# Optimization experiments

Hardware: AMD Instinct MI355X
Metric: run time of the kernel (lower is better)

Reference implementation:

```python
import jax, jax.numpy as jnp
import numpy as np

PI = float(np.pi)


def setup_inputs() -> dict:
    key = jax.random.key(0)
    k1, k2 = jax.random.split(key)
    src = jax.random.normal(k1, (32, 4, 512, 512), dtype=jnp.float32)
    fc2 = jax.random.normal(k2, (32, 7), dtype=jnp.float32)
    return {"src": src, "fc2": fc2}


def _build_mat(fc2):
    # Parameter extraction exactly as in the torch module.
    theta = jnp.clip(fc2[:, 0] * 0.3, -1.0, 1.0) * PI          # rotation angle
    scale = jnp.clip(fc2[:, 1:3] * 0.3 + 1.0, 0.0, 5.0)
    trans = fc2[:, 3:5] * 0.3
    shear = jnp.clip(fc2[:, 5:7] * 0.3, -1.0, 1.0) * PI
    sx, sy = scale[:, 0], scale[:, 1]
    tx, ty = trans[:, 0], trans[:, 1]
    shxy, shyx = shear[:, 0], shear[:, 1]
    c, s = jnp.cos(theta), jnp.sin(theta)
    z, o = jnp.zeros_like(c), jnp.ones_like(c)

    def m3(rows):  # rows: list of 3 lists of 3 (B,) scalars -> (B,3,3)
        return jnp.stack([jnp.stack(r, axis=-1) for r in rows], axis=-2)

    # Note: the torch code stacks rows at dim=2 (making the transpose) then
    # transposes (1,2) back, so the effective matrices are the ones as-written.
    rot = m3([[c, -s, z], [s, c, z], [z, z, o]])
    scl = m3([[sx, z, z], [z, sy, z], [z, z, o]])
    shr = m3([[o, shxy, z], [shyx, o, z], [z, z, o]])
    trn = m3([[o, z, tx], [z, o, ty], [z, z, o]])
    # mat = T @ Sh @ S @ R  (batched 3x3 matmuls)
    return trn @ shr @ scl @ rot


def _affine_grid(theta2x3, H, W):
    # F.affine_grid with align_corners=False (the torch default used here):
    # pixel centers map to x=(2w+1)/W-1, y=(2h+1)/H-1.
    xs = (2.0 * jnp.arange(W, dtype=jnp.float32) + 1.0) / W - 1.0  # (W,)
    ys = (2.0 * jnp.arange(H, dtype=jnp.float32) + 1.0) / H - 1.0  # (H,)
    base = jnp.stack([
        jnp.broadcast_to(xs[None, :], (H, W)),
        jnp.broadcast_to(ys[:, None], (H, W)),
        jnp.ones((H, W), dtype=jnp.float32),
    ], axis=-1)                                                     # (H,W,3)
    return jnp.einsum('bij,hwj->bhwi', theta2x3, base)              # (B,H,W,2)


def _grid_sample(src, grid):
    # bilinear, padding_mode='zeros', align_corners=False
    B, C, H, W = src.shape
    ix = ((grid[..., 0] + 1.0) * W - 1.0) * 0.5  # (B,H,W) source x coords
    iy = ((grid[..., 1] + 1.0) * H - 1.0) * 0.5
    x0 = jnp.floor(ix)
    y0 = jnp.floor(iy)
    wx = ix - x0  # frac weights
    wy = iy - y0
    x0i = x0.astype(jnp.int32)
    y0i = y0.astype(jnp.int32)

    def gather(img, xi, yi):  # img (C,H,W); xi,yi (H,W) int
        valid = ((xi >= 0) & (xi < W) & (yi >= 0) & (yi < H)).astype(img.dtype)
        v = img[:, jnp.clip(yi, 0, H - 1), jnp.clip(xi, 0, W - 1)]  # (C,H,W)
        return v * valid[None]

    def per_batch(img, x0i, y0i, wx, wy):
        v00 = gather(img, x0i, y0i)
        v01 = gather(img, x0i + 1, y0i)
        v10 = gather(img, x0i, y0i + 1)
        v11 = gather(img, x0i + 1, y0i + 1)
        return (v00 * (1 - wx) * (1 - wy) + v01 * wx * (1 - wy)
                + v10 * (1 - wx) * wy + v11 * wx * wy)

    return jax.vmap(per_batch)(src, x0i, y0i, wx, wy)


def reference(src, fc2):
    H, W = src.shape[2], src.shape[3]
    mat = _build_mat(fc2)                     # (B,3,3)
    inv_mat = jnp.linalg.inv(mat)             # (B,3,3)
    grid = _affine_grid(mat[:, :2, :], H, W)
    inv_grid = _affine_grid(inv_mat[:, :2, :], H, W)
    transformed = _grid_sample(src, grid)
    return transformed, mat, inv_mat, grid, inv_grid
```

## Files before the change

### kernel.cpp

```cpp
#include <hip/hip_runtime.h>

#define PI_F 3.14159265358979323846f

typedef float f32x4 __attribute__((ext_vector_type(4)));

__global__ void build_mats_kernel(const float* __restrict__ fc2,
                                  float* __restrict__ mat_out,
                                  float* __restrict__ inv_out,
                                  int B) {
    int b = blockIdx.x * blockDim.x + threadIdx.x;
    if (b >= B) return;
    const float* f = fc2 + b * 7;
    float theta = fminf(fmaxf(f[0] * 0.3f, -1.f), 1.f) * PI_F;
    float sx    = fminf(fmaxf(f[1] * 0.3f + 1.f, 0.f), 5.f);
    float sy    = fminf(fmaxf(f[2] * 0.3f + 1.f, 0.f), 5.f);
    float tx    = f[3] * 0.3f;
    float ty    = f[4] * 0.3f;
    float shxy  = fminf(fmaxf(f[5] * 0.3f, -1.f), 1.f) * PI_F;
    float shyx  = fminf(fmaxf(f[6] * 0.3f, -1.f), 1.f) * PI_F;

    float c = cosf(theta), s = sinf(theta);
    float m00 =  sx * c + shxy * sy * s;
    float m01 = -sx * s + shxy * sy * c;
    float m02 = tx;
    float m10 = shyx * sx * c + sy * s;
    float m11 = -shyx * sx * s + sy * c;
    float m12 = ty;

    float* m = mat_out + b * 9;
    m[0] = m00; m[1] = m01; m[2] = m02;
    m[3] = m10; m[4] = m11; m[5] = m12;
    m[6] = 0.f; m[7] = 0.f; m[8] = 1.f;

    float det = m00 * m11 - m01 * m10;
    float id  = 1.f / det;
    float i00 =  m11 * id, i01 = -m01 * id;
    float i10 = -m10 * id, i11 =  m00 * id;
    float i02 = -(i00 * m02 + i01 * m12);
    float i12 = -(i10 * m02 + i11 * m12);

    float* im = inv_out + b * 9;
    im[0] = i00; im[1] = i01; im[2] = i02;
    im[3] = i10; im[4] = i11; im[5] = i12;
    im[6] = 0.f; im[7] = 0.f; im[8] = 1.f;
}

__global__ __launch_bounds__(256) void grid_kernel(
    const float* __restrict__ mat,
    const float* __restrict__ inv_mat,
    float* __restrict__ grid_out,
    float* __restrict__ inv_grid_out)
{
    const int W = 512, H = 512;
    const int h = blockIdx.x;
    const int b = blockIdx.y;
    const int w = threadIdx.x * 2;

    float xs0 = (2.f * (float)w + 1.f) * (1.f / (float)W) - 1.f;
    float xs1 = xs0 + 2.f / (float)W;
    float ys  = (2.f * (float)h + 1.f) * (1.f / (float)H) - 1.f;

    const float* m  = mat + b * 9;
    const float* im = inv_mat + b * 9;

    float gx0  = m[0] * xs0 + (m[1] * ys + m[2]);
    float gy0  = m[3] * xs0 + (m[4] * ys + m[5]);
    float gx1  = m[0] * xs1 + (m[1] * ys + m[2]);
    float gy1  = m[3] * xs1 + (m[4] * ys + m[5]);
    float igx0 = im[0] * xs0 + (im[1] * ys + im[2]);
    float igy0 = im[3] * xs0 + (im[4] * ys + im[5]);
    float igx1 = im[0] * xs1 + (im[1] * ys + im[2]);
    float igy1 = im[3] * xs1 + (im[4] * ys + im[5]);

    size_t vec = ((size_t)b * H + h) * (W / 2) + threadIdx.x;
    f32x4 g  = {gx0, gy0, gx1, gy1};
    f32x4 ig = {igx0, igy0, igx1, igy1};
    __builtin_nontemporal_store(g,  (f32x4*)grid_out + vec);
    __builtin_nontemporal_store(ig, (f32x4*)inv_grid_out + vec);
}

__global__ __launch_bounds__(256) void sample_kernel(
    const float* __restrict__ src,
    const float* __restrict__ mat,
    float* __restrict__ transformed)
{
    const int W = 512, H = 512, C = 4;
    const int w = blockIdx.x * 16 + threadIdx.x;
    const int h = blockIdx.y * 16 + threadIdx.z * 4 + threadIdx.y;
    const int b = blockIdx.z;

    float xs = (2.f * (float)w + 1.f) * (1.f / (float)W) - 1.f;
    float ys = (2.f * (float)h + 1.f) * (1.f / (float)H) - 1.f;

    const float* m = mat + b * 9;
    float gx = m[0] * xs + (m[1] * ys + m[2]);
    float gy = m[3] * xs + (m[4] * ys + m[5]);

    float ix = ((gx + 1.f) * (float)W - 1.f) * 0.5f;
    float iy = ((gy + 1.f) * (float)H - 1.f) * 0.5f;
    float x0f = floorf(ix), y0f = floorf(iy);
    float wx = ix - x0f, wy = iy - y0f;
    int x0 = (int)x0f, y0 = (int)y0f;
    int x1 = x0 + 1,   y1 = y0 + 1;

    bool vx0 = (x0 >= 0) && (x0 < W);
    bool vx1 = (x1 >= 0) && (x1 < W);
    bool vy0 = (y0 >= 0) && (y0 < H);
    bool vy1 = (y1 >= 0) && (y1 < H);
    int cx0 = min(max(x0, 0), W - 1), cx1 = min(max(x1, 0), W - 1);
    int cy0 = min(max(y0, 0), H - 1), cy1 = min(max(y1, 0), H - 1);

    float w00 = (1.f - wx) * (1.f - wy) * ((vx0 && vy0) ? 1.f : 0.f);
    float w01 = wx * (1.f - wy)         * ((vx1 && vy0) ? 1.f : 0.f);
    float w10 = (1.f - wx) * wy         * ((vx0 && vy1) ? 1.f : 0.f);
    float w11 = wx * wy                 * ((vx1 && vy1) ? 1.f : 0.f);

    const float* sb = src + (size_t)b * C * H * W;
    int o00 = cy0 * W + cx0;
    int o01 = cy0 * W + cx1;
    int o10 = cy1 * W + cx0;
    int o11 = cy1 * W + cx1;

    #pragma unroll
    for (int c = 0; c < C; ++c) {
        const float* sc = sb + c * (H * W);
        float v = sc[o00] * w00 + sc[o01] * w01 + sc[o10] * w10 + sc[o11] * w11;
        __builtin_nontemporal_store(
            v, transformed + (((size_t)b * C + c) * H + h) * W + w);
    }
}

extern "C" void kernel_launch(void* const* d_in, const int* in_sizes, int n_in,
                              void* d_out, int out_size, void* d_ws, size_t ws_size,
                              hipStream_t stream) {
    const float* src = (const float*)d_in[0];
    const float* fc2 = (const float*)d_in[1];

    const int B = 32, C = 4, H = 512, W = 512;
    float* out = (float*)d_out;

    float* transformed  = out;
    float* mat_out      = out + (size_t)B * C * H * W;
    float* inv_out      = mat_out + (size_t)B * 9;
    float* grid_out     = inv_out + (size_t)B * 9;
    float* inv_grid_out = grid_out + (size_t)B * H * W * 2;

    build_mats_kernel<<<1, 64, 0, stream>>>(fc2, mat_out, inv_out, B);

    grid_kernel<<<dim3(H, B), 256, 0, stream>>>(mat_out, inv_out,
                                                grid_out, inv_grid_out);

    sample_kernel<<<dim3(W / 16, H / 16, B), dim3(16, 4, 4), 0, stream>>>(
        src, mat_out, transformed);
}
```

Before: 445.7 us.

## Stage source bounding box in LDS for bilinear sampling tiles

For each 16x16 output tile, the sample kernel computes the bounding box of the source coordinates the tile will read. If that box fits in a 2048-float-per-channel LDS buffer, the block loads it once into shared memory and does the four-tap gathers from LDS. Otherwise it falls back to direct global gathers. The goal is to cut scattered global reads and improve coalescing. The cost is an extra staging pass and a barrier, and tiles under large scale or shear transforms can load a mostly unused box or skip staging altogether.

```diff
diff --git a/kernel.cpp b/kernel.cpp
--- a/kernel.cpp
+++ b/kernel.cpp
@@ -84,17 +84,57 @@
     const float* __restrict__ mat,
     float* __restrict__ transformed)
 {
-    const int W = 512, H = 512, C = 4;
-    const int w = blockIdx.x * 16 + threadIdx.x;
-    const int h = blockIdx.y * 16 + threadIdx.z * 4 + threadIdx.y;
-    const int b = blockIdx.z;
+    const int W = 512, H = 512;
+    constexpr int CAP = 2048;
+    __shared__ float tile[4][CAP];
+
+    const int tx = threadIdx.x, ty = threadIdx.y;
+    const int w0 = blockIdx.x * 16, h0 = blockIdx.y * 16;
+    const int b  = blockIdx.z;
+    const int w = w0 + tx, h = h0 + ty;
+
+    const float* m = mat + b * 9;
+    const float m0 = m[0], m1 = m[1], m2 = m[2];
+    const float m3 = m[3], m4 = m[4], m5 = m[5];
+
+    float minix = 1e30f, maxix = -1e30f, miniy = 1e30f, maxiy = -1e30f;
+    #pragma unroll
+    for (int j = 0; j < 2; ++j) {
+        #pragma unroll
+        for (int i = 0; i < 2; ++i) {
+            float xs = (2.f * (float)(w0 + i * 15) + 1.f) * (1.f / (float)W) - 1.f;
+            float ys = (2.f * (float)(h0 + j * 15) + 1.f) * (1.f / (float)H) - 1.f;
+            float gx = m0 * xs + (m1 * ys + m2);
+            float gy = m3 * xs + (m4 * ys + m5);
+            float cix = ((gx + 1.f) * (float)W - 1.f) * 0.5f;
+            float ciy = ((gy + 1.f) * (float)H - 1.f) * 0.5f;
+            minix = fminf(minix, cix); maxix = fmaxf(maxix, cix);
+            miniy = fminf(miniy, ciy); maxiy = fmaxf(maxiy, ciy);
+        }
+    }
+    const int bx0 = min(max((int)floorf(minix) - 1, 0), W - 1);
+    const int bx1 = min(max((int)floorf(maxix) + 2, 0), W - 1);
+    const int by0 = min(max((int)floorf(miniy) - 1, 0), H - 1);
+    const int by1 = min(max((int)floorf(maxiy) + 2, 0), H - 1);
+    const int bw  = bx1 - bx0 + 1, bh = by1 - by0 + 1;
+    const int bwp = bw | 1;
+    const bool staged = (bh * bwp) <= CAP;
+
+    if (staged) {
+        #pragma unroll
+        for (int c = 0; c < 4; ++c) {
+            const float* sp = src + ((size_t)b * 4 + c) * H * W;
+            for (int yy = ty; yy < bh; yy += 16)
+                for (int xx = tx; xx < bw; xx += 16)
+                    tile[c][yy * bwp + xx] = sp[(by0 + yy) * W + (bx0 + xx)];
+        }
+        __syncthreads();
+    }
 
     float xs = (2.f * (float)w + 1.f) * (1.f / (float)W) - 1.f;
     float ys = (2.f * (float)h + 1.f) * (1.f / (float)H) - 1.f;
-
-    const float* m = mat + b * 9;
-    float gx = m[0] * xs + (m[1] * ys + m[2]);
-    float gy = m[3] * xs + (m[4] * ys + m[5]);
+    float gx = m0 * xs + (m1 * ys + m2);
+    float gy = m3 * xs + (m4 * ys + m5);
 
     float ix = ((gx + 1.f) * (float)W - 1.f) * 0.5f;
     float iy = ((gy + 1.f) * (float)H - 1.f) * 0.5f;
@@ -115,18 +155,32 @@
     float w10 = (1.f - wx) * wy         * ((vx0 && vy1) ? 1.f : 0.f);
     float w11 = wx * wy                 * ((vx1 && vy1) ? 1.f : 0.f);
 
-    const float* sb = src + (size_t)b * C * H * W;
-    int o00 = cy0 * W + cx0;
-    int o01 = cy0 * W + cx1;
-    int o10 = cy1 * W + cx0;
-    int o11 = cy1 * W + cx1;
-
-    #pragma unroll
-    for (int c = 0; c < C; ++c) {
-        const float* sc = sb + c * (H * W);
-        float v = sc[o00] * w00 + sc[o01] * w01 + sc[o10] * w10 + sc[o11] * w11;
-        __builtin_nontemporal_store(
-            v, transformed + (((size_t)b * C + c) * H + h) * W + w);
+    if (staged) {
+        int r0 = (cy0 - by0) * bwp - bx0;
+        int r1 = (cy1 - by0) * bwp - bx0;
+        int l00 = r0 + cx0, l01 = r0 + cx1;
+        int l10 = r1 + cx0, l11 = r1 + cx1;
+        #pragma unroll
+        for (int c = 0; c < 4; ++c) {
+            float v = tile[c][l00] * w00 + tile[c][l01] * w01
+                    + tile[c][l10] * w10 + tile[c][l11] * w11;
+            __builtin_nontemporal_store(
+                v, transformed + (((size_t)b * 4 + c) * H + h) * W + w);
+        }
+    } else {
+        const float* sb = src + (size_t)b * 4 * H * W;
+        int o00 = cy0 * W + cx0;
+        int o01 = cy0 * W + cx1;
+        int o10 = cy1 * W + cx0;
+        int o11 = cy1 * W + cx1;
+        #pragma unroll
+        for (int c = 0; c < 4; ++c) {
+            const float* sc = sb + c * (H * W);
+            float v = sc[o00] * w00 + sc[o01] * w01
+                    + sc[o10] * w10 + sc[o11] * w11;
+            __builtin_nontemporal_store(
+                v, transformed + (((size_t)b * 4 + c) * H + h) * W + w);
+        }
     }
 }
 
@@ -150,6 +204,6 @@
     grid_kernel<<<dim3(H, B), 256, 0, stream>>>(mat_out, inv_out,
                                                 grid_out, inv_grid_out);
 
-    sample_kernel<<<dim3(W / 16, H / 16, B), dim3(16, 4, 4), 0, stream>>>(
+    sample_kernel<<<dim3(W / 16, H / 16, B), dim3(16, 16, 1), 0, stream>>>(
         src, mat_out, transformed);
 }
```

Measured after the change: 544.9 us. 1.22x slower.

## Fuse grid generation and bilinear sampling into one interleaved launch

Applied to the files above, without the earlier changes.

Merges the grid-writing kernel and the sampling kernel into a single 1D launch. Every fifth block writes two grid rows for both grids, and the other four blocks do sampling. The sample tiles are remapped so each wave covers an 8x8 pixel patch, which should improve gather locality. The aim is to cut launch and tail overhead and to overlap the store-heavy grid writes with the gather-heavy sampling, at the cost of divergent block roles and extra index arithmetic.

```diff
diff --git a/kernel.cpp b/kernel.cpp
--- a/kernel.cpp
+++ b/kernel.cpp
@@ -45,54 +45,62 @@
     im[6] = 0.f; im[7] = 0.f; im[8] = 1.f;
 }
 
-__global__ __launch_bounds__(256) void grid_kernel(
+__global__ __launch_bounds__(256) void fused_kernel(
+    const float* __restrict__ src,
     const float* __restrict__ mat,
     const float* __restrict__ inv_mat,
+    float* __restrict__ transformed,
     float* __restrict__ grid_out,
     float* __restrict__ inv_grid_out)
 {
     const int W = 512, H = 512;
-    const int h = blockIdx.x;
-    const int b = blockIdx.y;
-    const int w = threadIdx.x * 2;
+    const int bid = blockIdx.x;
+    const int q = bid / 5, r = bid - q * 5;
 
-    float xs0 = (2.f * (float)w + 1.f) * (1.f / (float)W) - 1.f;
-    float xs1 = xs0 + 2.f / (float)W;
-    float ys  = (2.f * (float)h + 1.f) * (1.f / (float)H) - 1.f;
+    if (r == 4) {
+        const int widx = q;
+        const int b  = widx >> 8;
+        const int rp = widx & 255;
+        const int t  = threadIdx.x;
 
-    const float* m  = mat + b * 9;
-    const float* im = inv_mat + b * 9;
+        const float* m  = mat + b * 9;
+        const float* im = inv_mat + b * 9;
+        const float m0 = m[0],  m1 = m[1],  m2 = m[2];
+        const float m3 = m[3],  m4 = m[4],  m5 = m[5];
+        const float i0 = im[0], i1 = im[1], i2 = im[2];
+        const float i3 = im[3], i4 = im[4], i5 = im[5];
 
-    float gx0  = m[0] * xs0 + (m[1] * ys + m[2]);
-    float gy0  = m[3] * xs0 + (m[4] * ys + m[5]);
-    float gx1  = m[0] * xs1 + (m[1] * ys + m[2]);
-    float gy1  = m[3] * xs1 + (m[4] * ys + m[5]);
-    float igx0 = im[0] * xs0 + (im[1] * ys + im[2]);
-    float igy0 = im[3] * xs0 + (im[4] * ys + im[5]);
-    float igx1 = im[0] * xs1 + (im[1] * ys + im[2]);
-    float igy1 = im[3] * xs1 + (im[4] * ys + im[5]);
+        float xs0 = (2.f * (float)(2 * t) + 1.f) * (1.f / (float)W) - 1.f;
+        float xs1 = xs0 + 2.f / (float)W;
 
-    size_t vec = ((size_t)b * H + h) * (W / 2) + threadIdx.x;
-    f32x4 g  = {gx0, gy0, gx1, gy1};
-    f32x4 ig = {igx0, igy0, igx1, igy1};
-    __builtin_nontemporal_store(g,  (f32x4*)grid_out + vec);
-    __builtin_nontemporal_store(ig, (f32x4*)inv_grid_out + vec);
-}
+        #pragma unroll
+        for (int rr = 0; rr < 2; ++rr) {
+            int h = rp * 2 + rr;
+            float ys = (2.f * (float)h + 1.f) * (1.f / (float)H) - 1.f;
+            f32x4 g  = {m0 * xs0 + (m1 * ys + m2), m3 * xs0 + (m4 * ys + m5),
+                        m0 * xs1 + (m1 * ys + m2), m3 * xs1 + (m4 * ys + m5)};
+            f32x4 ig = {i0 * xs0 + (i1 * ys + i2), i3 * xs0 + (i4 * ys + i5),
+                        i0 * xs1 + (i1 * ys + i2), i3 * xs1 + (i4 * ys + i5)};
+            size_t vec = ((size_t)b * H + h) * (W / 2) + t;
+            __builtin_nontemporal_store(g,  (f32x4*)grid_out + vec);
+            __builtin_nontemporal_store(ig, (f32x4*)inv_grid_out + vec);
+        }
+        return;
+    }
 
-__global__ __launch_bounds__(256) void sample_kernel(
-    const float* __restrict__ src,
-    const float* __restrict__ mat,
-    float* __restrict__ transformed)
-{
-    const int W = 512, H = 512, C = 4;
-    const int w = blockIdx.x * 16 + threadIdx.x;
-    const int h = blockIdx.y * 16 + threadIdx.z * 4 + threadIdx.y;
-    const int b = blockIdx.z;
+    const int sidx = q * 4 + r;
+    const int b   = sidx >> 10;
+    const int rem = sidx & 1023;
+    const int w0 = (rem & 31) * 16, h0 = (rem >> 5) * 16;
 
+    const int t    = threadIdx.x;
+    const int wave = t >> 6, lane = t & 63;
+    const int w = w0 + (wave & 1) * 8 + (lane & 7);
+    const int h = h0 + (wave >> 1) * 8 + (lane >> 3);
+
+    const float* m = mat + b * 9;
     float xs = (2.f * (float)w + 1.f) * (1.f / (float)W) - 1.f;
     float ys = (2.f * (float)h + 1.f) * (1.f / (float)H) - 1.f;
-
-    const float* m = mat + b * 9;
     float gx = m[0] * xs + (m[1] * ys + m[2]);
     float gy = m[3] * xs + (m[4] * ys + m[5]);
 
@@ -115,18 +123,18 @@
     float w10 = (1.f - wx) * wy         * ((vx0 && vy1) ? 1.f : 0.f);
     float w11 = wx * wy                 * ((vx1 && vy1) ? 1.f : 0.f);
 
-    const float* sb = src + (size_t)b * C * H * W;
+    const float* sb = src + (size_t)b * 4 * H * W;
     int o00 = cy0 * W + cx0;
     int o01 = cy0 * W + cx1;
     int o10 = cy1 * W + cx0;
     int o11 = cy1 * W + cx1;
 
     #pragma unroll
-    for (int c = 0; c < C; ++c) {
+    for (int c = 0; c < 4; ++c) {
         const float* sc = sb + c * (H * W);
         float v = sc[o00] * w00 + sc[o01] * w01 + sc[o10] * w10 + sc[o11] * w11;
         __builtin_nontemporal_store(
-            v, transformed + (((size_t)b * C + c) * H + h) * W + w);
+            v, transformed + (((size_t)b * 4 + c) * H + h) * W + w);
     }
 }
 
@@ -147,9 +155,6 @@
 
     build_mats_kernel<<<1, 64, 0, stream>>>(fc2, mat_out, inv_out, B);
 
-    grid_kernel<<<dim3(H, B), 256, 0, stream>>>(mat_out, inv_out,
-                                                grid_out, inv_grid_out);
-
-    sample_kernel<<<dim3(W / 16, H / 16, B), dim3(16, 4, 4), 0, stream>>>(
-        src, mat_out, transformed);
+    fused_kernel<<<dim3(40960), dim3(256), 0, stream>>>(
+        src, mat_out, inv_out, transformed, grid_out, inv_grid_out);
 }
```

Result: faster. 408.7 us (-8.3%).
